# Performance work log

Hardware: AMD Instinct MI355X
Metric: run time of the kernel (lower is better)

Reference implementation:

```python
import jax, jax.numpy as jnp
import numpy as np

T, B, DIM, N_STATE = 2048, 16, 1024, 1024
EPS = 1e-6


def setup_inputs() -> dict:
    key = jax.random.key(0)
    kx, kk, kv, kq = jax.random.split(key, 4)
    xavier = np.sqrt(2.0 / (N_STATE + DIM)).astype(np.float32)
    return {
        "x": jax.random.normal(kx, (T, B, DIM), dtype=jnp.float32),
        "W_k": jax.random.normal(kk, (N_STATE, DIM), dtype=jnp.float32) * xavier,
        "W_v": jax.random.normal(kv, (N_STATE, DIM), dtype=jnp.float32) * xavier,
        "W_q": jax.random.normal(kq, (N_STATE, DIM), dtype=jnp.float32) * xavier,
    }


def reference(x, W_k, W_v, W_q):
    # Projections for all timesteps at once: [T, B, n]
    k = jnp.einsum("tbd,nd->tbn", x, W_k)
    v = jnp.einsum("tbd,nd->tbn", x, W_v)
    q = jnp.einsum("tbd,nd->tbn", x, W_q)
    # L2-normalize k per (t, b) over the state dim (matches k_t.norm(dim=-1))
    k_norm = k / (jnp.linalg.norm(k, axis=-1, keepdims=True) + EPS)

    Tn, Bn, n = k.shape
    S0 = jnp.zeros((Bn, n), dtype=x.dtype)

    def step(S, inp):
        k_t, v_t, q_t = inp
        # Delta update with OUTPUT gating + tanh nonlinearity
        S_new = jnp.tanh(S * (1.0 - k_t * k_t) + v_t * k_t)
        Sq = S_new * q_t
        out = Sq * jax.nn.silu(Sq)
        return S_new, out

    S_final, output = jax.lax.scan(step, S0, (k_norm, v, q))
    return output, S_final
```

## Files before the change

### kernel.cpp

```cpp
#include <hip/hip_runtime.h>
#include <hip/hip_fp16.h>

#define T_STEPS 2048
#define BATCH 16
#define DIMD 1024
#define NSTATE 1024
#define MROWS (T_STEPS * BATCH)
#define NCH (BATCH * NSTATE)
#define NKT (DIMD / 32)

typedef _Float16 f16x8 __attribute__((ext_vector_type(8)));
typedef float f32x4 __attribute__((ext_vector_type(4)));

#define GAS(p) ((const __attribute__((address_space(1))) void*)(p))
#define LAS(p) ((__attribute__((address_space(3))) void*)(p))

__global__ void cvt_kernel(const float* __restrict__ src, _Float16* __restrict__ dst, int n8) {
  int i = blockIdx.x * blockDim.x + threadIdx.x;
  if (i >= n8) return;
  const float4* s4 = (const float4*)src;
  float4 a = s4[(size_t)i * 2];
  float4 b = s4[(size_t)i * 2 + 1];
  f16x8 o;
  o[0] = (_Float16)a.x; o[1] = (_Float16)a.y; o[2] = (_Float16)a.z; o[3] = (_Float16)a.w;
  o[4] = (_Float16)b.x; o[5] = (_Float16)b.y; o[6] = (_Float16)b.z; o[7] = (_Float16)b.w;
  *((f16x8*)dst + i) = o;
}

__global__ __launch_bounds__(512, 2) void gemm_kernel(const _Float16* __restrict__ A,
                                                      const _Float16* __restrict__ Wcat,
                                                      _Float16* __restrict__ KVQt,
                                                      float* __restrict__ rnpart) {
  __shared__ _Float16 As[2][256 * 32];
  __shared__ _Float16 Bs[2][256 * 32];
  const int tid = threadIdx.x;
  const int lane = tid & 63;
  const int w = tid >> 6;
  const int wr = w >> 2;
  const int wc = w & 3;

  const int bid = blockIdx.x;
  const int swz = (bid & 7) * 192 + (bid >> 3);
  const int mat = swz >> 9;
  const int rem = swz & 511;
  const int tileM = rem >> 2;
  const int tileN = rem & 3;

  const _Float16* Ag = A + (size_t)tileM * 256 * DIMD;
  const _Float16* Bg = Wcat + (size_t)mat * NSTATE * DIMD + (size_t)tileN * 256 * DIMD;

  const int s0 = w * 128 + lane;
  const int s1 = s0 + 64;
  const int sr0 = s0 >> 2, sc0 = ((s0 & 3) ^ ((s0 >> 3) & 3)) * 8;
  const int sr1 = s1 >> 2, sc1 = ((s1 & 3) ^ ((s1 >> 3) & 3)) * 8;

#define STAGE(buf, TT)                                                                  \
  do {                                                                                  \
    const int kk = (TT) * 32;                                                           \
    __builtin_amdgcn_global_load_lds(GAS(Ag + (size_t)sr0 * DIMD + kk + sc0),           \
                                     LAS(&As[buf][s0 * 8]), 16, 0, 0);                  \
    __builtin_amdgcn_global_load_lds(GAS(Ag + (size_t)sr1 * DIMD + kk + sc1),           \
                                     LAS(&As[buf][s1 * 8]), 16, 0, 0);                  \
    __builtin_amdgcn_global_load_lds(GAS(Bg + (size_t)sr0 * DIMD + kk + sc0),           \
                                     LAS(&Bs[buf][s0 * 8]), 16, 0, 0);                  \
    __builtin_amdgcn_global_load_lds(GAS(Bg + (size_t)sr1 * DIMD + kk + sc1),           \
                                     LAS(&Bs[buf][s1 * 8]), 16, 0, 0);                  \
  } while (0)

  f32x4 acc[8][4];
#pragma unroll
  for (int m = 0; m < 8; ++m)
#pragma unroll
    for (int n = 0; n < 4; ++n)
      acc[m][n] = (f32x4){0.f, 0.f, 0.f, 0.f};

  STAGE(0, 0);
  STAGE(1, 1);

  const int fr = lane & 15;
  const int cbp = ((lane >> 4) ^ ((fr >> 1) & 3)) * 8;

#pragma unroll 2
  for (int T = 0; T < NKT; ++T) {
    const int buf = T & 1;
    __builtin_amdgcn_sched_barrier(0);
    if (T < NKT - 2) {
      asm volatile("s_waitcnt vmcnt(4)" ::: "memory");
    } else {
      asm volatile("s_waitcnt vmcnt(0)" ::: "memory");
    }
    __builtin_amdgcn_s_barrier();
    __builtin_amdgcn_sched_barrier(0);

    f16x8 af[8], bf[4];
#pragma unroll
    for (int m = 0; m < 8; ++m)
      af[m] = *(const f16x8*)(&As[buf][(wr * 128 + m * 16 + fr) * 32 + cbp]);
#pragma unroll
    for (int n = 0; n < 4; ++n)
      bf[n] = *(const f16x8*)(&Bs[buf][(wc * 64 + n * 16 + fr) * 32 + cbp]);

    __builtin_amdgcn_s_setprio(1);
#pragma unroll
    for (int m = 0; m < 8; ++m)
#pragma unroll
      for (int n = 0; n < 2; ++n)
        acc[m][n] = __builtin_amdgcn_mfma_f32_16x16x32_f16(af[m], bf[n], acc[m][n], 0, 0, 0);
    __builtin_amdgcn_s_setprio(0);

    asm volatile("s_waitcnt lgkmcnt(0)" ::: "memory");
    __builtin_amdgcn_sched_barrier(0);
    __builtin_amdgcn_s_barrier();
    __builtin_amdgcn_sched_barrier(0);

    if (T < NKT - 2) STAGE(buf, T + 2);
    __builtin_amdgcn_s_setprio(1);
#pragma unroll
    for (int m = 0; m < 8; ++m)
#pragma unroll
      for (int n = 2; n < 4; ++n)
        acc[m][n] = __builtin_amdgcn_mfma_f32_16x16x32_f16(af[m], bf[n], acc[m][n], 0, 0, 0);
    __builtin_amdgcn_s_setprio(0);
  }

  const int cc = lane & 15;
  const int l4 = lane >> 4;
  _Float16* Cb = KVQt + (size_t)mat * ((size_t)MROWS * NSTATE) +
                 (size_t)(tileM * 2 + wr) * ((size_t)NCH * 8);
#pragma unroll
  for (int n = 0; n < 4; ++n)
#pragma unroll
    for (int j = 0; j < 4; ++j) {
      f16x8 pk;
#pragma unroll
      for (int m = 0; m < 8; ++m) pk[m] = (_Float16)acc[m][n][j];
      const int b = l4 * 4 + j;
      const int gcol = tileN * 256 + wc * 64 + n * 16 + cc;
      *(f16x8*)(Cb + ((size_t)(b * 1024 + gcol)) * 8) = pk;
    }

  if (mat == 0) {
#pragma unroll
    for (int m = 0; m < 8; ++m)
#pragma unroll
      for (int j = 0; j < 4; ++j) {
        float p = 0.f;
#pragma unroll
        for (int n = 0; n < 4; ++n) p += acc[m][n][j] * acc[m][n][j];
        p += __shfl_xor(p, 1);
        p += __shfl_xor(p, 2);
        p += __shfl_xor(p, 4);
        p += __shfl_xor(p, 8);
        if (cc == 0) {
          const int gr = tileM * 256 + wr * 128 + m * 16 + l4 * 4 + j;
          rnpart[(size_t)(tileN * 4 + wc) * MROWS + gr] = p;
        }
      }
  }
}

__global__ void rnfin_kernel(const float* __restrict__ part, float* __restrict__ rn) {
  const int r = blockIdx.x * 256 + threadIdx.x;
  float s = 0.f;
#pragma unroll
  for (int i = 0; i < 16; ++i) s += part[(size_t)i * MROWS + r];
  rn[r] = 1.f / (sqrtf(s) + 1e-6f);
}

#define STILE 16

#define LOADT(P, t0in)                                                        \
  do {                                                                        \
    const int tc = ((t0in) < T_STEPS) ? (t0in) : (T_STEPS - STILE);           \
    const size_t o0 = ((size_t)(tc >> 3) * NCH + c) * 8;                      \
    P##k0 = *(const f16x8*)(Kt + o0);                                         \
    P##k1 = *(const f16x8*)(Kt + o0 + (size_t)NCH * 8);                       \
    P##v0 = *(const f16x8*)(Vt + o0);                                         \
    P##v1 = *(const f16x8*)(Vt + o0 + (size_t)NCH * 8);                       \
    P##q0 = *(const f16x8*)(Qt + o0);                                         \
    P##q1 = *(const f16x8*)(Qt + o0 + (size_t)NCH * 8);                       \
    _Pragma("unroll") for (int i = 0; i < STILE; ++i)                         \
        P##r[i] = rn[(tc + i) * 16 + b];                                      \
  } while (0)

#define STEPT(P, t0)                                                          \
  do {                                                                        \
    float a2[STILE], b2[STILE], qf[STILE];                                    \
    _Pragma("unroll") for (int i = 0; i < STILE; ++i) {                       \
      float kf = (float)((i < 8) ? P##k0[i & 7] : P##k1[i & 7]);              \
      float vf = (float)((i < 8) ? P##v0[i & 7] : P##v1[i & 7]);              \
      float kn = kf * P##r[i];                                                \
      a2[i] = L2E2 - (L2E2 * kn) * kn;                                        \
      b2[i] = L2E2 * (vf * kn);                                               \
      qf[i] = (float)((i < 8) ? P##q0[i & 7] : P##q1[i & 7]);                 \
    }                                                                         \
    _Pragma("unroll") for (int i = 0; i < STILE; ++i) {                       \
      float u = fmaf(S, a2[i], b2[i]);                                        \
      float e = __builtin_amdgcn_exp2f(u);                                    \
      float r = __builtin_amdgcn_rcpf(e + 1.f);                               \
      S = fmaf(-2.f, r, 1.f);                                                 \
      float z = S * qf[i];                                                    \
      float sg = __builtin_amdgcn_rcpf(1.f + __builtin_amdgcn_exp2f(-L2E * z)); \
      out[(size_t)((t0) + i) * NCH + c] = z * z * sg;                         \
    }                                                                         \
  } while (0)

__global__ __launch_bounds__(256) void scan_kernel(const _Float16* __restrict__ Kt,
                                                   const _Float16* __restrict__ Vt,
                                                   const _Float16* __restrict__ Qt,
                                                   const float* __restrict__ rn,
                                                   float* __restrict__ out,
                                                   float* __restrict__ sfin) {
  const int c = blockIdx.x * 256 + threadIdx.x;
  const int b = c >> 10;
  constexpr float L2E2 = 2.8853900817779268f;
  constexpr float L2E = 1.4426950408889634f;
  float S = 0.f;
  f16x8 Ak0, Ak1, Av0, Av1, Aq0, Aq1;
  f16x8 Bk0, Bk1, Bv0, Bv1, Bq0, Bq1;
  float Ar[STILE], Br[STILE];

  LOADT(A, 0);
  for (int t0 = 0; t0 < T_STEPS; t0 += 2 * STILE) {
    LOADT(B, t0 + STILE);
    STEPT(A, t0);
    LOADT(A, t0 + 2 * STILE);
    STEPT(B, t0 + STILE);
  }
  sfin[c] = S;
}

extern "C" void kernel_launch(void* const* d_in, const int* in_sizes, int n_in,
                              void* d_out, int out_size, void* d_ws, size_t ws_size,
                              hipStream_t stream) {
  const float* x = (const float*)d_in[0];
  const float* Wk = (const float*)d_in[1];
  const float* Wv = (const float*)d_in[2];
  const float* Wq = (const float*)d_in[3];

  char* ws = (char*)d_ws;
  _Float16* xh = (_Float16*)ws;
  _Float16* Wh = (_Float16*)(ws + 67108864ull);
  _Float16* KVQt = (_Float16*)(ws + 67108864ull + 6291456ull);
  float* rnpart = (float*)(ws + 67108864ull + 6291456ull + 201326592ull);
  float* rn = (float*)(ws + 67108864ull + 6291456ull + 201326592ull + 2097152ull);

  int n8x = MROWS * DIMD / 8;
  cvt_kernel<<<(n8x + 255) / 256, 256, 0, stream>>>(x, xh, n8x);
  int n8w = NSTATE * DIMD / 8;
  cvt_kernel<<<(n8w + 255) / 256, 256, 0, stream>>>(Wk, Wh, n8w);
  cvt_kernel<<<(n8w + 255) / 256, 256, 0, stream>>>(Wv, Wh + (size_t)NSTATE * DIMD, n8w);
  cvt_kernel<<<(n8w + 255) / 256, 256, 0, stream>>>(Wq, Wh + (size_t)2 * NSTATE * DIMD, n8w);

  gemm_kernel<<<1536, 512, 0, stream>>>(xh, Wh, KVQt, rnpart);

  rnfin_kernel<<<MROWS / 256, 256, 0, stream>>>(rnpart, rn);

  const _Float16* Kt = KVQt;
  const _Float16* Vt = KVQt + (size_t)MROWS * NSTATE;
  const _Float16* Qt = KVQt + 2ull * MROWS * NSTATE;
  float* outp = (float*)d_out;
  scan_kernel<<<NCH / 256, 256, 0, stream>>>(Kt, Vt, Qt, rn, outp, outp + (size_t)MROWS * NSTATE);
}
```

Before: 434.7 us.

## Restructure GEMM to 64-wide K tiles, fuse weight casts, transpose norms, shrink scan blocks

The GEMM now stages 64-wide K slices into a single 128KB LDS buffer split into halves. It runs with one block per CU and is fully unrolled over 16 K tiles, with next-tile loads interleaved between MFMA halves. This aims to cut barrier count and improve load/compute overlap, but it lowers occupancy. The three weight-conversion launches are merged into one 2D-grid kernel. The reciprocal norms are stored transposed so the scan can read them with vector loads, and the scan uses 64-thread blocks to spread work across more CUs.

```diff
diff --git a/kernel.cpp b/kernel.cpp
--- a/kernel.cpp
+++ b/kernel.cpp
@@ -7,7 +7,6 @@
 #define NSTATE 1024
 #define MROWS (T_STEPS * BATCH)
 #define NCH (BATCH * NSTATE)
-#define NKT (DIMD / 32)
 
 typedef _Float16 f16x8 __attribute__((ext_vector_type(8)));
 typedef float f32x4 __attribute__((ext_vector_type(4)));
@@ -27,17 +26,29 @@
   *((f16x8*)dst + i) = o;
 }
 
-__global__ __launch_bounds__(512, 2) void gemm_kernel(const _Float16* __restrict__ A,
+__global__ void cvtW_kernel(const float* __restrict__ wk, const float* __restrict__ wv,
+                            const float* __restrict__ wq, _Float16* __restrict__ dst) {
+  const float* src = blockIdx.y == 0 ? wk : blockIdx.y == 1 ? wv : wq;
+  int i = blockIdx.x * blockDim.x + threadIdx.x;
+  const float4* s4 = (const float4*)src;
+  float4 a = s4[(size_t)i * 2];
+  float4 b = s4[(size_t)i * 2 + 1];
+  f16x8 o;
+  o[0] = (_Float16)a.x; o[1] = (_Float16)a.y; o[2] = (_Float16)a.z; o[3] = (_Float16)a.w;
+  o[4] = (_Float16)b.x; o[5] = (_Float16)b.y; o[6] = (_Float16)b.z; o[7] = (_Float16)b.w;
+  *((f16x8*)dst + (size_t)blockIdx.y * (NSTATE * DIMD / 8) + i) = o;
+}
+
+__global__ __launch_bounds__(512, 1) void gemm_kernel(const _Float16* __restrict__ A,
                                                       const _Float16* __restrict__ Wcat,
                                                       _Float16* __restrict__ KVQt,
                                                       float* __restrict__ rnpart) {
-  __shared__ _Float16 As[2][256 * 32];
-  __shared__ _Float16 Bs[2][256 * 32];
+  __shared__ _Float16 lds[65536];
   const int tid = threadIdx.x;
   const int lane = tid & 63;
   const int w = tid >> 6;
-  const int wr = w >> 2;
-  const int wc = w & 3;
+  const int wm = w >> 2;
+  const int wn = w & 3;
 
   const int bid = blockIdx.x;
   const int swz = (bid & 7) * 192 + (bid >> 3);
@@ -49,22 +60,18 @@
   const _Float16* Ag = A + (size_t)tileM * 256 * DIMD;
   const _Float16* Bg = Wcat + (size_t)mat * NSTATE * DIMD + (size_t)tileN * 256 * DIMD;
 
-  const int s0 = w * 128 + lane;
-  const int s1 = s0 + 64;
+  const int s0 = tid, s1 = tid + 512;
   const int sr0 = s0 >> 2, sc0 = ((s0 & 3) ^ ((s0 >> 3) & 3)) * 8;
   const int sr1 = s1 >> 2, sc1 = ((s1 & 3) ^ ((s1 >> 3) & 3)) * 8;
 
-#define STAGE(buf, TT)                                                                  \
+#define STAGE_H(G, buf, hb, TT, h)                                                      \
   do {                                                                                  \
-    const int kk = (TT) * 32;                                                           \
-    __builtin_amdgcn_global_load_lds(GAS(Ag + (size_t)sr0 * DIMD + kk + sc0),           \
-                                     LAS(&As[buf][s0 * 8]), 16, 0, 0);                  \
-    __builtin_amdgcn_global_load_lds(GAS(Ag + (size_t)sr1 * DIMD + kk + sc1),           \
-                                     LAS(&As[buf][s1 * 8]), 16, 0, 0);                  \
-    __builtin_amdgcn_global_load_lds(GAS(Bg + (size_t)sr0 * DIMD + kk + sc0),           \
-                                     LAS(&Bs[buf][s0 * 8]), 16, 0, 0);                  \
-    __builtin_amdgcn_global_load_lds(GAS(Bg + (size_t)sr1 * DIMD + kk + sc1),           \
-                                     LAS(&Bs[buf][s1 * 8]), 16, 0, 0);                  \
+    __builtin_amdgcn_global_load_lds(                                                   \
+        GAS(G + (size_t)sr0 * DIMD + (TT) * 64 + (h) * 32 + sc0),                       \
+        LAS(lds + (buf) * 32768 + ((hb) + (h)) * 8192 + s0 * 8), 16, 0, 0);             \
+    __builtin_amdgcn_global_load_lds(                                                   \
+        GAS(G + (size_t)sr1 * DIMD + (TT) * 64 + (h) * 32 + sc1),                       \
+        LAS(lds + (buf) * 32768 + ((hb) + (h)) * 8192 + s1 * 8), 16, 0, 0);             \
   } while (0)
 
   f32x4 acc[8][4];
@@ -74,59 +81,75 @@
     for (int n = 0; n < 4; ++n)
       acc[m][n] = (f32x4){0.f, 0.f, 0.f, 0.f};
 
-  STAGE(0, 0);
-  STAGE(1, 1);
+  STAGE_H(Ag, 0, 0, 0, 0);
+  STAGE_H(Bg, 0, 2, 0, 0);
+  STAGE_H(Ag, 0, 0, 0, 1);
+  STAGE_H(Bg, 0, 2, 0, 1);
 
   const int fr = lane & 15;
   const int cbp = ((lane >> 4) ^ ((fr >> 1) & 3)) * 8;
 
-#pragma unroll 2
-  for (int T = 0; T < NKT; ++T) {
-    const int buf = T & 1;
-    __builtin_amdgcn_sched_barrier(0);
-    if (T < NKT - 2) {
-      asm volatile("s_waitcnt vmcnt(4)" ::: "memory");
-    } else {
-      asm volatile("s_waitcnt vmcnt(0)" ::: "memory");
-    }
-    __builtin_amdgcn_s_barrier();
-    __builtin_amdgcn_sched_barrier(0);
-
-    f16x8 af[8], bf[4];
-#pragma unroll
-    for (int m = 0; m < 8; ++m)
-      af[m] = *(const f16x8*)(&As[buf][(wr * 128 + m * 16 + fr) * 32 + cbp]);
-#pragma unroll
-    for (int n = 0; n < 4; ++n)
-      bf[n] = *(const f16x8*)(&Bs[buf][(wc * 64 + n * 16 + fr) * 32 + cbp]);
-
-    __builtin_amdgcn_s_setprio(1);
-#pragma unroll
-    for (int m = 0; m < 8; ++m)
-#pragma unroll
-      for (int n = 0; n < 2; ++n)
-        acc[m][n] = __builtin_amdgcn_mfma_f32_16x16x32_f16(af[m], bf[n], acc[m][n], 0, 0, 0);
-    __builtin_amdgcn_s_setprio(0);
-
-    asm volatile("s_waitcnt lgkmcnt(0)" ::: "memory");
-    __builtin_amdgcn_sched_barrier(0);
-    __builtin_amdgcn_s_barrier();
-    __builtin_amdgcn_sched_barrier(0);
-
-    if (T < NKT - 2) STAGE(buf, T + 2);
-    __builtin_amdgcn_s_setprio(1);
-#pragma unroll
-    for (int m = 0; m < 8; ++m)
-#pragma unroll
-      for (int n = 2; n < 4; ++n)
-        acc[m][n] = __builtin_amdgcn_mfma_f32_16x16x32_f16(af[m], bf[n], acc[m][n], 0, 0, 0);
-    __builtin_amdgcn_s_setprio(0);
-  }
+#define KTILE(T)                                                                        \
+  do {                                                                                  \
+    const int buf = (T) & 1, bufn = buf ^ 1;                                            \
+    f16x8 a0[8], b0[4], a1[8], b1[4];                                                   \
+                    \
+    asm volatile("s_waitcnt vmcnt(4)" ::: "memory");                                    \
+    __builtin_amdgcn_s_barrier();                                                       \
+    __builtin_amdgcn_sched_barrier(0);                                                  \
+    if ((T) + 1 < 16) STAGE_H(Ag, bufn, 0, (T) + 1, 0);                                 \
+    _Pragma("unroll") for (int m = 0; m < 8; ++m)                                       \
+        a0[m] = *(const f16x8*)(lds + buf * 32768 + 0 * 8192 +                          \
+                                (wm * 128 + m * 16 + fr) * 32 + cbp);                   \
+    _Pragma("unroll") for (int n = 0; n < 4; ++n)                                       \
+        b0[n] = *(const f16x8*)(lds + buf * 32768 + 2 * 8192 +                          \
+                                (wn * 64 + n * 16 + fr) * 32 + cbp);                    \
+    __builtin_amdgcn_s_setprio(1);                                                      \
+    _Pragma("unroll") for (int m = 0; m < 8; ++m) _Pragma("unroll") for (int n = 0; n < 2; ++n) \
+        acc[m][n] = __builtin_amdgcn_mfma_f32_16x16x32_f16(a0[m], b0[n], acc[m][n], 0, 0, 0); \
+    __builtin_amdgcn_s_setprio(0);                                                      \
+                                         \
+    if ((T) + 1 < 16) STAGE_H(Bg, bufn, 2, (T) + 1, 0);                                 \
+    __builtin_amdgcn_s_setprio(1);                                                      \
+    _Pragma("unroll") for (int m = 0; m < 8; ++m) _Pragma("unroll") for (int n = 2; n < 4; ++n) \
+        acc[m][n] = __builtin_amdgcn_mfma_f32_16x16x32_f16(a0[m], b0[n], acc[m][n], 0, 0, 0); \
+    __builtin_amdgcn_s_setprio(0);                                                      \
+                    \
+    if ((T) + 1 < 16) {                                                                 \
+      asm volatile("s_waitcnt vmcnt(4)" ::: "memory");                                  \
+    } else {                                                                            \
+      asm volatile("s_waitcnt vmcnt(0)" ::: "memory");                                  \
+    }                                                                                   \
+    __builtin_amdgcn_s_barrier();                                                       \
+    __builtin_amdgcn_sched_barrier(0);                                                  \
+    if ((T) + 1 < 16) STAGE_H(Ag, bufn, 0, (T) + 1, 1);                                 \
+    _Pragma("unroll") for (int m = 0; m < 8; ++m)                                       \
+        a1[m] = *(const f16x8*)(lds + buf * 32768 + 1 * 8192 +                          \
+                                (wm * 128 + m * 16 + fr) * 32 + cbp);                   \
+    _Pragma("unroll") for (int n = 0; n < 4; ++n)                                       \
+        b1[n] = *(const f16x8*)(lds + buf * 32768 + 3 * 8192 +                          \
+                                (wn * 64 + n * 16 + fr) * 32 + cbp);                    \
+    __builtin_amdgcn_s_setprio(1);                                                      \
+    _Pragma("unroll") for (int m = 0; m < 8; ++m) _Pragma("unroll") for (int n = 0; n < 2; ++n) \
+        acc[m][n] = __builtin_amdgcn_mfma_f32_16x16x32_f16(a1[m], b1[n], acc[m][n], 0, 0, 0); \
+    __builtin_amdgcn_s_setprio(0);                                                      \
+                                         \
+    if ((T) + 1 < 16) STAGE_H(Bg, bufn, 2, (T) + 1, 1);                                 \
+    __builtin_amdgcn_s_setprio(1);                                                      \
+    _Pragma("unroll") for (int m = 0; m < 8; ++m) _Pragma("unroll") for (int n = 2; n < 4; ++n) \
+        acc[m][n] = __builtin_amdgcn_mfma_f32_16x16x32_f16(a1[m], b1[n], acc[m][n], 0, 0, 0); \
+    __builtin_amdgcn_s_setprio(0);                                                      \
+  } while (0)
+
+  KTILE(0);  KTILE(1);  KTILE(2);  KTILE(3);
+  KTILE(4);  KTILE(5);  KTILE(6);  KTILE(7);
+  KTILE(8);  KTILE(9);  KTILE(10); KTILE(11);
+  KTILE(12); KTILE(13); KTILE(14); KTILE(15);
 
   const int cc = lane & 15;
   const int l4 = lane >> 4;
   _Float16* Cb = KVQt + (size_t)mat * ((size_t)MROWS * NSTATE) +
-                 (size_t)(tileM * 2 + wr) * ((size_t)NCH * 8);
+                 (size_t)(tileM * 2 + wm) * ((size_t)NCH * 8);
 #pragma unroll
   for (int n = 0; n < 4; ++n)
 #pragma unroll
@@ -135,7 +158,7 @@
 #pragma unroll
       for (int m = 0; m < 8; ++m) pk[m] = (_Float16)acc[m][n][j];
       const int b = l4 * 4 + j;
-      const int gcol = tileN * 256 + wc * 64 + n * 16 + cc;
+      const int gcol = tileN * 256 + wn * 64 + n * 16 + cc;
       *(f16x8*)(Cb + ((size_t)(b * 1024 + gcol)) * 8) = pk;
     }
 
@@ -152,19 +175,19 @@
         p += __shfl_xor(p, 4);
         p += __shfl_xor(p, 8);
         if (cc == 0) {
-          const int gr = tileM * 256 + wr * 128 + m * 16 + l4 * 4 + j;
-          rnpart[(size_t)(tileN * 4 + wc) * MROWS + gr] = p;
+          const int gr = tileM * 256 + wm * 128 + m * 16 + l4 * 4 + j;
+          rnpart[(size_t)(tileN * 4 + wn) * MROWS + gr] = p;
         }
       }
   }
 }
 
-__global__ void rnfin_kernel(const float* __restrict__ part, float* __restrict__ rn) {
+__global__ void rnfin_kernel(const float* __restrict__ part, float* __restrict__ rnT) {
   const int r = blockIdx.x * 256 + threadIdx.x;
   float s = 0.f;
 #pragma unroll
   for (int i = 0; i < 16; ++i) s += part[(size_t)i * MROWS + r];
-  rn[r] = 1.f / (sqrtf(s) + 1e-6f);
+  rnT[(r & 15) * T_STEPS + (r >> 4)] = 1.f / (sqrtf(s) + 1e-6f);
 }
 
 #define STILE 16
@@ -179,8 +202,10 @@
     P##v1 = *(const f16x8*)(Vt + o0 + (size_t)NCH * 8);                       \
     P##q0 = *(const f16x8*)(Qt + o0);                                         \
     P##q1 = *(const f16x8*)(Qt + o0 + (size_t)NCH * 8);                       \
-    _Pragma("unroll") for (int i = 0; i < STILE; ++i)                         \
-        P##r[i] = rn[(tc + i) * 16 + b];                                      \
+    P##r0 = *(const f32x4*)(rnT + bb + tc);                                   \
+    P##r1 = *(const f32x4*)(rnT + bb + tc + 4);                               \
+    P##r2 = *(const f32x4*)(rnT + bb + tc + 8);                               \
+    P##r3 = *(const f32x4*)(rnT + bb + tc + 12);                              \
   } while (0)
 
 #define STEPT(P, t0)                                                          \
@@ -189,7 +214,10 @@
     _Pragma("unroll") for (int i = 0; i < STILE; ++i) {                       \
       float kf = (float)((i < 8) ? P##k0[i & 7] : P##k1[i & 7]);              \
       float vf = (float)((i < 8) ? P##v0[i & 7] : P##v1[i & 7]);              \
-      float kn = kf * P##r[i];                                                \
+      float rv = (i < 4) ? P##r0[i & 3]                                       \
+               : (i < 8) ? P##r1[i & 3]                                       \
+               : (i < 12) ? P##r2[i & 3] : P##r3[i & 3];                      \
+      float kn = kf * rv;                                                     \
       a2[i] = L2E2 - (L2E2 * kn) * kn;                                        \
       b2[i] = L2E2 * (vf * kn);                                               \
       qf[i] = (float)((i < 8) ? P##q0[i & 7] : P##q1[i & 7]);                 \
@@ -205,20 +233,20 @@
     }                                                                         \
   } while (0)
 
-__global__ __launch_bounds__(256) void scan_kernel(const _Float16* __restrict__ Kt,
-                                                   const _Float16* __restrict__ Vt,
-                                                   const _Float16* __restrict__ Qt,
-                                                   const float* __restrict__ rn,
-                                                   float* __restrict__ out,
-                                                   float* __restrict__ sfin) {
-  const int c = blockIdx.x * 256 + threadIdx.x;
-  const int b = c >> 10;
+__global__ __launch_bounds__(64) void scan_kernel(const _Float16* __restrict__ Kt,
+                                                  const _Float16* __restrict__ Vt,
+                                                  const _Float16* __restrict__ Qt,
+                                                  const float* __restrict__ rnT,
+                                                  float* __restrict__ out,
+                                                  float* __restrict__ sfin) {
+  const int c = blockIdx.x * 64 + threadIdx.x;
+  const int bb = (c >> 10) * T_STEPS;
   constexpr float L2E2 = 2.8853900817779268f;
   constexpr float L2E = 1.4426950408889634f;
   float S = 0.f;
   f16x8 Ak0, Ak1, Av0, Av1, Aq0, Aq1;
   f16x8 Bk0, Bk1, Bv0, Bv1, Bq0, Bq1;
-  float Ar[STILE], Br[STILE];
+  f32x4 Ar0, Ar1, Ar2, Ar3, Br0, Br1, Br2, Br3;
 
   LOADT(A, 0);
   for (int t0 = 0; t0 < T_STEPS; t0 += 2 * STILE) {
@@ -243,22 +271,19 @@
   _Float16* Wh = (_Float16*)(ws + 67108864ull);
   _Float16* KVQt = (_Float16*)(ws + 67108864ull + 6291456ull);
   float* rnpart = (float*)(ws + 67108864ull + 6291456ull + 201326592ull);
-  float* rn = (float*)(ws + 67108864ull + 6291456ull + 201326592ull + 2097152ull);
+  float* rnT = (float*)(ws + 67108864ull + 6291456ull + 201326592ull + 2097152ull);
 
   int n8x = MROWS * DIMD / 8;
   cvt_kernel<<<(n8x + 255) / 256, 256, 0, stream>>>(x, xh, n8x);
-  int n8w = NSTATE * DIMD / 8;
-  cvt_kernel<<<(n8w + 255) / 256, 256, 0, stream>>>(Wk, Wh, n8w);
-  cvt_kernel<<<(n8w + 255) / 256, 256, 0, stream>>>(Wv, Wh + (size_t)NSTATE * DIMD, n8w);
-  cvt_kernel<<<(n8w + 255) / 256, 256, 0, stream>>>(Wq, Wh + (size_t)2 * NSTATE * DIMD, n8w);
+  cvtW_kernel<<<dim3(NSTATE * DIMD / 8 / 256, 3), 256, 0, stream>>>(Wk, Wv, Wq, Wh);
 
   gemm_kernel<<<1536, 512, 0, stream>>>(xh, Wh, KVQt, rnpart);
 
-  rnfin_kernel<<<MROWS / 256, 256, 0, stream>>>(rnpart, rn);
+  rnfin_kernel<<<MROWS / 256, 256, 0, stream>>>(rnpart, rnT);
 
   const _Float16* Kt = KVQt;
   const _Float16* Vt = KVQt + (size_t)MROWS * NSTATE;
   const _Float16* Qt = KVQt + 2ull * MROWS * NSTATE;
   float* outp = (float*)d_out;
-  scan_kernel<<<NCH / 256, 256, 0, stream>>>(Kt, Vt, Qt, rn, outp, outp + (size_t)MROWS * NSTATE);
-}
+  scan_kernel<<<NCH / 64, 64, 0, stream>>>(Kt, Vt, Qt, rnT, outp, outp + (size_t)MROWS * NSTATE);
+}
```

Result: no change. 431.8 us (-0.7%).
